# Kernel optimization log

Hardware: AMD Instinct MI355X
Metric: run time of the kernel (lower is better)

The kernel has to match this reference:

```python
import jax, jax.numpy as jnp
import numpy as np

B, S, H, HD = 2, 2048, 16, 128
HID = H * HD            # 2048
FF = 4 * HID            # 8192
ROT = int(HD * 0.25)    # 32 rotary dims (rotary_pct=0.25)
EPS = 1e-5
ROPE_BASE = 10000.0


def _layernorm(x, g, b):
    mu = jnp.mean(x, axis=-1, keepdims=True)
    var = jnp.mean(jnp.square(x - mu), axis=-1, keepdims=True)
    return (x - mu) * jax.lax.rsqrt(var + EPS) * g + b


def _rope_cos_sin(seq_len, dim, dtype):
    inv_freq = 1.0 / (ROPE_BASE ** (np.arange(0, dim, 2, dtype=np.float32) / dim))
    t = np.arange(seq_len, dtype=np.float32)
    freqs = np.outer(t, inv_freq)              # [S, dim/2]
    emb = np.concatenate([freqs, freqs], -1)   # [S, dim]
    return jnp.asarray(np.cos(emb), dtype), jnp.asarray(np.sin(emb), dtype)


def _apply_rope(x, cos, sin):
    # x: [B, H, S, ROT]; GPTNeoX rotate_half
    half = x.shape[-1] // 2
    x1, x2 = x[..., :half], x[..., half:]
    rot = jnp.concatenate([-x2, x1], axis=-1)
    return x * cos[None, None, :, :] + rot * sin[None, None, :, :]


def setup_inputs() -> dict:
    key = jax.random.key(0)
    ks = jax.random.split(key, 8)
    f = jnp.float32
    return {
        "hidden_states": jax.random.normal(ks[0], (B, S, HID), f),
        "ln1_g": jnp.ones((HID,), f), "ln1_b": jnp.zeros((HID,), f),
        "ln2_g": jnp.ones((HID,), f), "ln2_b": jnp.zeros((HID,), f),
        "W_qkv": jax.random.normal(ks[1], (HID, 3 * HID), f) * 0.02,
        "b_qkv": jnp.zeros((3 * HID,), f),
        "W_o": jax.random.normal(ks[2], (HID, HID), f) * 0.02,
        "b_o": jnp.zeros((HID,), f),
        "W_fc": jax.random.normal(ks[3], (HID, FF), f) * 0.02,
        "b_fc": jnp.zeros((FF,), f),
        "W_proj": jax.random.normal(ks[4], (FF, HID), f) * 0.02,
        "b_proj": jnp.zeros((HID,), f),
    }


def reference(hidden_states, ln1_g, ln1_b, ln2_g, ln2_b,
              W_qkv, b_qkv, W_o, b_o, W_fc, b_fc, W_proj, b_proj):
    dtype = hidden_states.dtype
    x = _layernorm(hidden_states, ln1_g, ln1_b)

    # fused QKV, GPTNeoX per-head interleaved layout [B,S,H,3*HD]
    qkv = (x @ W_qkv + b_qkv).reshape(B, S, H, 3 * HD)
    q = jnp.transpose(qkv[..., :HD], (0, 2, 1, 3))          # [B,H,S,HD]
    k = jnp.transpose(qkv[..., HD:2 * HD], (0, 2, 1, 3))
    v = jnp.transpose(qkv[..., 2 * HD:], (0, 2, 1, 3))

    cos, sin = _rope_cos_sin(S, ROT, dtype)
    q = jnp.concatenate([_apply_rope(q[..., :ROT], cos, sin), q[..., ROT:]], -1)
    k = jnp.concatenate([_apply_rope(k[..., :ROT], cos, sin), k[..., ROT:]], -1)

    # eager attention: scores / sqrt(hd), causal mask-fill, softmax, matmul
    scale = 1.0 / jnp.sqrt(jnp.asarray(HD, dtype))
    scores = jnp.einsum("bhqd,bhkd->bhqk", q, k) * scale
    causal = jnp.tril(jnp.ones((S, S), bool))
    scores = jnp.where(causal, scores, jnp.finfo(dtype).min)
    weights = jax.nn.softmax(scores, axis=-1)
    ctx = jnp.einsum("bhqk,bhkd->bhqd", weights, v)          # [B,H,S,HD]
    ctx = jnp.transpose(ctx, (0, 2, 1, 3)).reshape(B, S, HID)
    attn_out = ctx @ W_o + b_o

    # parallel residual: mlp(ln2(h)) + attn(ln1(h)) + h
    m = _layernorm(hidden_states, ln2_g, ln2_b)
    mlp_out = jax.nn.gelu(m @ W_fc + b_fc, approximate=False) @ W_proj + b_proj
    return mlp_out + attn_out + hidden_states
```

## Files before the change

### kernel.cpp

```cpp
#include <hip/hip_runtime.h>
#include <hip/hip_bf16.h>
#include <math.h>

#define BDIM 2
#define SDIM 2048
#define HDIM 16
#define HD 128
#define HID 2048
#define FFD 8192
#define NTOK (BDIM*SDIM)
#define QKVW (3*HID)

typedef __hip_bfloat16 bf16;
typedef __attribute__((ext_vector_type(8))) short short8;
typedef __attribute__((ext_vector_type(4))) short short4_;
typedef __attribute__((ext_vector_type(4))) float floatx4;

__device__ inline short bfbits(float f) {
  bf16 h = __float2bfloat16(f);
  short s;
  __builtin_memcpy(&s, &h, 2);
  return s;
}

__device__ inline float fast_erf(float x) {
  float ax = fabsf(x);
  float t = __builtin_amdgcn_rcpf(1.0f + 0.3275911f * ax);
  float p = t * (0.254829592f + t * (-0.284496736f + t * (1.421413741f
          + t * (-1.453152027f + t * 1.061405429f))));
  float e = __expf(-ax * ax);
  float r = 1.0f - p * e;
  return copysignf(r, x);
}

__global__ __launch_bounds__(256) void transpose_cvt(
    const float* __restrict__ W, bf16* __restrict__ Wt, int K, int N)
{
  __shared__ float tile[32][33];
  int n0 = blockIdx.x * 32, k0 = blockIdx.y * 32;
  int tx = threadIdx.x, ty = threadIdx.y;
  #pragma unroll
  for (int r = ty; r < 32; r += 8)
    tile[r][tx] = W[(size_t)(k0 + r) * N + n0 + tx];
  __syncthreads();
  #pragma unroll
  for (int r = ty; r < 32; r += 8)
    Wt[(size_t)(n0 + r) * K + k0 + tx] = __float2bfloat16(tile[tx][r]);
}

__global__ __launch_bounds__(256) void ln_both(
    const float* __restrict__ x,
    const float* __restrict__ g1, const float* __restrict__ b1,
    const float* __restrict__ g2, const float* __restrict__ b2,
    bf16* __restrict__ o1, bf16* __restrict__ o2)
{
  int row = blockIdx.x;
  int tid = threadIdx.x;
  const float4* xr = (const float4*)(x + (size_t)row * HID);
  float4 va = xr[tid], vb = xr[tid + 256];
  float s = va.x + va.y + va.z + va.w + vb.x + vb.y + vb.z + vb.w;
  float q = va.x*va.x + va.y*va.y + va.z*va.z + va.w*va.w
          + vb.x*vb.x + vb.y*vb.y + vb.z*vb.z + vb.w*vb.w;
  #pragma unroll
  for (int off = 1; off < 64; off <<= 1) {
    s += __shfl_xor(s, off);
    q += __shfl_xor(q, off);
  }
  __shared__ float red[8];
  int wave = tid >> 6;
  if ((tid & 63) == 0) { red[wave] = s; red[4 + wave] = q; }
  __syncthreads();
  s = red[0] + red[1] + red[2] + red[3];
  q = red[4] + red[5] + red[6] + red[7];
  float mu = s * (1.0f / HID);
  float var = q * (1.0f / HID) - mu * mu;
  float rs = rsqrtf(var + 1e-5f);

  const float4* g1v = (const float4*)g1; const float4* b1v = (const float4*)b1;
  const float4* g2v = (const float4*)g2; const float4* b2v = (const float4*)b2;
  short4_* o1v = (short4_*)(o1 + (size_t)row * HID);
  short4_* o2v = (short4_*)(o2 + (size_t)row * HID);
  #pragma unroll
  for (int p = 0; p < 2; ++p) {
    int e = tid + p * 256;
    float4 xv = (p == 0) ? va : vb;
    float4 gv = g1v[e], bv = b1v[e];
    short4_ pk;
    pk[0] = bfbits((xv.x - mu) * rs * gv.x + bv.x);
    pk[1] = bfbits((xv.y - mu) * rs * gv.y + bv.y);
    pk[2] = bfbits((xv.z - mu) * rs * gv.z + bv.z);
    pk[3] = bfbits((xv.w - mu) * rs * gv.w + bv.w);
    o1v[e] = pk;
    gv = g2v[e]; bv = b2v[e];
    pk[0] = bfbits((xv.x - mu) * rs * gv.x + bv.x);
    pk[1] = bfbits((xv.y - mu) * rs * gv.y + bv.y);
    pk[2] = bfbits((xv.z - mu) * rs * gv.z + bv.z);
    pk[3] = bfbits((xv.w - mu) * rs * gv.w + bv.w);
    o2v[e] = pk;
  }
}

template<int EPI, int BM>
__global__ __launch_bounds__(512, 2) void gemm2p(
    const bf16* __restrict__ A, const bf16* __restrict__ Bt,
    const float* __restrict__ bias,
    float* __restrict__ Cf, bf16* __restrict__ Cb,
    const bf16* __restrict__ r1b, const float* __restrict__ r2,
    int M, int N, int K)
{
  constexpr int NI = BM / 32;
  __shared__ bf16 SA[2][BM * 64];
  __shared__ bf16 SB[2][256 * 64];
  const int tid = threadIdx.x;
  const int wave = tid >> 6, lane = tid & 63;
  const int quad = lane >> 4, l16 = lane & 15;
  const int wr = wave >> 2, wc = wave & 3;
  const int n0 = blockIdx.x * 256, m0 = blockIdx.y * BM;

  const int stg_r = tid >> 3;
  const int stg_c = ((tid & 7) ^ ((tid >> 3) & 7)) << 3;
  const bf16* stgA = A + (size_t)(m0 + stg_r) * K + stg_c;
  const bf16* stgB = Bt + (size_t)(n0 + stg_r) * K + stg_c;

  floatx4 acc[NI][4];
  #pragma unroll
  for (int i = 0; i < NI; ++i)
    #pragma unroll
    for (int j = 0; j < 4; ++j) acc[i][j] = (floatx4)0.0f;

  const int KT = K >> 6;

#define STAGE_2P(KT1, BUF) {                                                   \
  const bf16* ga_ = stgA + (size_t)(KT1) * 64;                                 \
  const bf16* gb_ = stgB + (size_t)(KT1) * 64;                                 \
  _Pragma("unroll")                                                            \
  for (int s_ = 0; s_ < BM / 64; ++s_)                                         \
    __builtin_amdgcn_global_load_lds(                                          \
        (const __attribute__((address_space(1))) void*)(ga_ + (size_t)s_ * 64 * K), \
        (__attribute__((address_space(3))) void*)&SA[BUF][s_ * 4096 + wave * 512], 16, 0, 0); \
  _Pragma("unroll")                                                            \
  for (int s_ = 0; s_ < 4; ++s_)                                               \
    __builtin_amdgcn_global_load_lds(                                          \
        (const __attribute__((address_space(1))) void*)(gb_ + (size_t)s_ * 64 * K), \
        (__attribute__((address_space(3))) void*)&SB[BUF][s_ * 4096 + wave * 512], 16, 0, 0); }

  STAGE_2P(0, 0);
  __syncthreads();

  for (int kt = 0; kt < KT; ++kt) {
    const int cur = kt & 1;
    if (kt + 1 < KT) STAGE_2P(kt + 1, cur ^ 1);
    const bf16* as_ = &SA[cur][0];
    const bf16* bs_ = &SB[cur][0];
    #pragma unroll
    for (int kc = 0; kc < 2; ++kc) {
      const int csw = (((kc * 4 + quad) ^ (l16 & 7)) << 3);
      short8 av[NI], bv[4];
      #pragma unroll
      for (int i = 0; i < NI; ++i)
        av[i] = *(const short8*)&as_[(wr * (BM / 2) + i * 16 + l16) * 64 + csw];
      #pragma unroll
      for (int j = 0; j < 4; ++j)
        bv[j] = *(const short8*)&bs_[(wc * 64 + j * 16 + l16) * 64 + csw];
      #pragma unroll
      for (int i = 0; i < NI; ++i)
        #pragma unroll
        for (int j = 0; j < 4; ++j)
          acc[i][j] = __builtin_amdgcn_mfma_f32_16x16x32_bf16(av[i], bv[j], acc[i][j], 0, 0, 0);
    }
    __syncthreads();
  }
#undef STAGE_2P

  #pragma unroll
  for (int i = 0; i < NI; ++i) {
    #pragma unroll
    for (int j = 0; j < 4; ++j) {
      int col = n0 + wc * 64 + j * 16 + l16;
      float bsv = bias[col];
      #pragma unroll
      for (int r = 0; r < 4; ++r) {
        int row = m0 + wr * (BM / 2) + i * 16 + quad * 4 + r;
        size_t idx = (size_t)row * N + col;
        float v = acc[i][j][r] + bsv;
        if (EPI == 1) {
          v = 0.5f * v * (1.0f + fast_erf(v * 0.70710678118654752f));
          Cb[idx] = __float2bfloat16(v);
        } else if (EPI == 2) {
          Cf[idx] = v + __bfloat162float(r1b[idx]) + r2[idx];
        } else {
          Cb[idx] = __float2bfloat16(v);
        }
      }
    }
  }
}

__global__ __launch_bounds__(256) void rope_vt(
    bf16* __restrict__ qkv, bf16* __restrict__ vT)
{
  int bh = blockIdx.x, s0 = blockIdx.y * 32;
  int b = bh >> 4, h = bh & 15;
  int tid = threadIdx.x;
  __shared__ bf16 vs[32][136];
  const float qsc = 0.12751740f;

  for (int idx = tid; idx < 512; idx += 256) {
    int sl = idx >> 4, d = idx & 15;
    int s = s0 + sl;
    bf16* base = qkv + (size_t)(b * SDIM + s) * QKVW + h * 384;
    float fr = (float)s * expf(-(float)d * 0.5756462732485114f);
    float c = cosf(fr), sn = sinf(fr);
    float q1 = __bfloat162float(base[d]);
    float q2 = __bfloat162float(base[d + 16]);
    float k1 = __bfloat162float(base[128 + d]);
    float k2 = __bfloat162float(base[128 + d + 16]);
    base[d]        = __float2bfloat16(qsc * (q1 * c - q2 * sn));
    base[d + 16]   = __float2bfloat16(qsc * (q2 * c + q1 * sn));
    base[128 + d]      = __float2bfloat16(k1 * c - k2 * sn);
    base[128 + d + 16] = __float2bfloat16(k2 * c + k1 * sn);
  }
  for (int idx = tid; idx < 32 * 96; idx += 256) {
    int sl = idx / 96, d = 32 + idx % 96;
    bf16* base = qkv + (size_t)(b * SDIM + s0 + sl) * QKVW + h * 384;
    base[d] = __float2bfloat16(qsc * __bfloat162float(base[d]));
  }

  for (int idx = tid; idx < 32 * 128; idx += 256) {
    int sl = idx >> 7, d = idx & 127;
    vs[sl][d] = qkv[(size_t)(b * SDIM + s0 + sl) * QKVW + h * 384 + 256 + d];
  }
  __syncthreads();
  for (int idx = tid; idx < 32 * 128; idx += 256) {
    int d = idx >> 5, sl = idx & 31;
    vT[((size_t)bh * HD + d) * SDIM + s0 + sl] = vs[sl][d];
  }
}

#define LOAD_K(KB, K0) { \
  int krow_ = (K0); \
  _Pragma("unroll") for (int nh_ = 0; nh_ < 2; ++nh_) \
    _Pragma("unroll") for (int c_ = 0; c_ < 4; ++c_) \
      KB[nh_*4+c_] = *(const short8*)&Kb[(size_t)(krow_ + nh_*16 + l16) * QKVW + c_*32 + quad*8]; }

#define SOFTMAX(S0, S1, MR, LR, OO, ROWQ, DOMASK, K0, SLOT) { \
  if (DOMASK) { \
    _Pragma("unroll") for (int r_ = 0; r_ < 4; ++r_) { \
      int row_ = (ROWQ) + quad*4 + r_; \
      S0[r_] = ((K0) + l16 <= row_) ? S0[r_] : -1e30f; \
      S1[r_] = ((K0) + 16 + l16 <= row_) ? S1[r_] : -1e30f; } } \
  _Pragma("unroll") for (int r_ = 0; r_ < 4; ++r_) { \
    float mx_ = fmaxf(S0[r_], S1[r_]); \
    mx_ = fmaxf(mx_, __shfl_xor(mx_, 1)); \
    mx_ = fmaxf(mx_, __shfl_xor(mx_, 2)); \
    mx_ = fmaxf(mx_, __shfl_xor(mx_, 4)); \
    mx_ = fmaxf(mx_, __shfl_xor(mx_, 8)); \
    float mnew_ = fmaxf(MR[r_], mx_); \
    float alpha_ = __builtin_amdgcn_exp2f(MR[r_] - mnew_); \
    MR[r_] = mnew_; \
    S0[r_] = __builtin_amdgcn_exp2f(S0[r_] - mnew_); \
    S1[r_] = __builtin_amdgcn_exp2f(S1[r_] - mnew_); \
    float sm_ = S0[r_] + S1[r_]; \
    sm_ += __shfl_xor(sm_, 1); sm_ += __shfl_xor(sm_, 2); \
    sm_ += __shfl_xor(sm_, 4); sm_ += __shfl_xor(sm_, 8); \
    LR[r_] = LR[r_] * alpha_ + sm_; \
    _Pragma("unroll") for (int d_ = 0; d_ < 8; ++d_) OO[d_][r_] *= alpha_; \
    Ps[wave][SLOT][quad*4 + r_][l16]      = __float2bfloat16(S0[r_]); \
    Ps[wave][SLOT][quad*4 + r_][16 + l16] = __float2bfloat16(S1[r_]); } }

#define FLASH_ITER(IT, KC, KN) { \
  const int k0_ = (IT) * 32; \
  const int k0n_ = ((IT) + 1 < nk) ? k0_ + 32 : 0; \
  LOAD_K(KN, k0n_); \
  short8 vbuf_[8]; \
  _Pragma("unroll") for (int d_ = 0; d_ < 8; ++d_) \
    vbuf_[d_] = *(const short8*)&Vb[(size_t)(d_*16 + l16) * SDIM + k0_ + quad*8]; \
  floatx4 scB_[2]; scB_[0] = (floatx4)0.0f; scB_[1] = (floatx4)0.0f; \
  _Pragma("unroll") for (int c_ = 0; c_ < 4; ++c_) { \
    scB_[0] = __builtin_amdgcn_mfma_f32_16x16x32_bf16(aqB[c_], KC[c_],   scB_[0], 0,0,0); \
    scB_[1] = __builtin_amdgcn_mfma_f32_16x16x32_bf16(aqB[c_], KC[4+c_], scB_[1], 0,0,0); } \
  const bool actA_ = (k0_ <= qa + 15); \
  floatx4 scA_[2]; scA_[0] = (floatx4)0.0f; scA_[1] = (floatx4)0.0f; \
  if (actA_) { \
    _Pragma("unroll") for (int c_ = 0; c_ < 4; ++c_) { \
      scA_[0] = __builtin_amdgcn_mfma_f32_16x16x32_bf16(aqA[c_], KC[c_],   scA_[0], 0,0,0); \
      scA_[1] = __builtin_amdgcn_mfma_f32_16x16x32_bf16(aqA[c_], KC[4+c_], scA_[1], 0,0,0); } } \
  SOFTMAX(scB_[0], scB_[1], mB, lB, oB, qb, (k0_ + 32 >= kmax), k0_, 0); \
  if (actA_) { \
    SOFTMAX(scA_[0], scA_[1], mA, lA, oA, qa, (k0_ + 32 > qa + 15), k0_, 1); \
    short8 pfB_ = *(const short8*)&Ps[wave][0][l16][quad*8]; \
    short8 pfA_ = *(const short8*)&Ps[wave][1][l16][quad*8]; \
    _Pragma("unroll") for (int d_ = 0; d_ < 8; ++d_) { \
      oB[d_] = __builtin_amdgcn_mfma_f32_16x16x32_bf16(pfB_, vbuf_[d_], oB[d_], 0,0,0); \
      oA[d_] = __builtin_amdgcn_mfma_f32_16x16x32_bf16(pfA_, vbuf_[d_], oA[d_], 0,0,0); } \
  } else { \
    short8 pfB_ = *(const short8*)&Ps[wave][0][l16][quad*8]; \
    _Pragma("unroll") for (int d_ = 0; d_ < 8; ++d_) \
      oB[d_] = __builtin_amdgcn_mfma_f32_16x16x32_bf16(pfB_, vbuf_[d_], oB[d_], 0,0,0); } }

__global__ __launch_bounds__(256) void flash_attn(
    const bf16* __restrict__ qkv, const bf16* __restrict__ vT,
    bf16* __restrict__ ctx)
{
  int bh = blockIdx.x;
  int b = bh >> 4, h = bh & 15;
  int tid = threadIdx.x;
  int wave = tid >> 6, lane = tid & 63;
  int quad = lane >> 4, l16 = lane & 15;
  int p = blockIdx.y * 4 + wave;
  int qa = 16 * p;
  int qb = SDIM - 16 * (p + 1);
  int kmax = qb + 16;
  int nk = (kmax + 31) >> 5;
  const bf16* Qb = qkv + (size_t)b * SDIM * QKVW + h * 384;
  const bf16* Kb = Qb + 128;
  const bf16* Vb = vT + (size_t)bh * HD * SDIM;
  __shared__ bf16 Ps[4][2][16][32];

  short8 aqA[4], aqB[4];
  #pragma unroll
  for (int c = 0; c < 4; ++c) {
    aqA[c] = *(const short8*)&Qb[(size_t)(qa + l16) * QKVW + c * 32 + quad * 8];
    aqB[c] = *(const short8*)&Qb[(size_t)(qb + l16) * QKVW + c * 32 + quad * 8];
  }

  floatx4 oA[8], oB[8];
  #pragma unroll
  for (int d = 0; d < 8; ++d) { oA[d] = (floatx4)0.0f; oB[d] = (floatx4)0.0f; }
  float mA[4] = {-INFINITY, -INFINITY, -INFINITY, -INFINITY};
  float mB[4] = {-INFINITY, -INFINITY, -INFINITY, -INFINITY};
  float lA[4] = {0.0f, 0.0f, 0.0f, 0.0f};
  float lB[4] = {0.0f, 0.0f, 0.0f, 0.0f};

  short8 kb0[8], kb1[8];
  LOAD_K(kb0, 0);
  for (int it = 0; it < nk; it += 2) {
    FLASH_ITER(it, kb0, kb1);
    if (it + 1 < nk) { FLASH_ITER(it + 1, kb1, kb0); }
  }

  float rlA[4], rlB[4];
  #pragma unroll
  for (int r = 0; r < 4; ++r) { rlA[r] = 1.0f / lA[r]; rlB[r] = 1.0f / lB[r]; }
  #pragma unroll
  for (int d = 0; d < 8; ++d) {
    #pragma unroll
    for (int r = 0; r < 4; ++r) {
      int rowA = qa + quad * 4 + r;
      int rowB = qb + quad * 4 + r;
      ctx[((size_t)b * SDIM + rowA) * HID + h * HD + d * 16 + l16] =
          __float2bfloat16(oA[d][r] * rlA[r]);
      ctx[((size_t)b * SDIM + rowB) * HID + h * HD + d * 16 + l16] =
          __float2bfloat16(oB[d][r] * rlB[r]);
    }
  }
}

extern "C" void kernel_launch(void* const* d_in, const int* in_sizes, int n_in,
                              void* d_out, int out_size, void* d_ws, size_t ws_size,
                              hipStream_t stream) {
  const float* hidden = (const float*)d_in[0];
  const float* ln1g = (const float*)d_in[1];
  const float* ln1b = (const float*)d_in[2];
  const float* ln2g = (const float*)d_in[3];
  const float* ln2b = (const float*)d_in[4];
  const float* Wqkv = (const float*)d_in[5];
  const float* bqkv = (const float*)d_in[6];
  const float* Wo   = (const float*)d_in[7];
  const float* bo   = (const float*)d_in[8];
  const float* Wfc  = (const float*)d_in[9];
  const float* bfc  = (const float*)d_in[10];
  const float* Wproj= (const float*)d_in[11];
  const float* bproj= (const float*)d_in[12];

  char* ws = (char*)d_ws;
  const size_t SZ_WQKV = (size_t)QKVW * HID * 2;
  const size_t SZ_WO   = (size_t)HID * HID * 2;
  const size_t SZ_WFC  = (size_t)FFD * HID * 2;
  const size_t SZ_WPROJ= (size_t)HID * FFD * 2;
  const size_t SZ_ACT  = (size_t)NTOK * HID * 2;
  const size_t SZ_QKV  = (size_t)NTOK * QKVW * 2;

  bf16* wqkvT = (bf16*)(ws + 0);
  bf16* woT   = (bf16*)(ws + SZ_WQKV);
  bf16* wfcT  = (bf16*)(ws + SZ_WQKV + SZ_WO);
  bf16* wprojT= (bf16*)(ws + SZ_WQKV + SZ_WO + SZ_WFC);
  char* actbase = ws + SZ_WQKV + SZ_WO + SZ_WFC + SZ_WPROJ;
  bf16* xln   = (bf16*)(actbase);
  bf16* mln   = (bf16*)(actbase + SZ_ACT);
  bf16* qkvb  = (bf16*)(actbase + 2 * SZ_ACT);
  bf16* vT    = (bf16*)(actbase + 2 * SZ_ACT + SZ_QKV);
  bf16* ctx   = xln;
  bf16* attnb = wqkvT;
  bf16* hfc   = qkvb;

  dim3 tblk(32, 8);
  transpose_cvt<<<dim3(QKVW / 32, HID / 32), tblk, 0, stream>>>(Wqkv, wqkvT, HID, QKVW);
  transpose_cvt<<<dim3(HID / 32, HID / 32), tblk, 0, stream>>>(Wo, woT, HID, HID);
  transpose_cvt<<<dim3(FFD / 32, HID / 32), tblk, 0, stream>>>(Wfc, wfcT, HID, FFD);
  transpose_cvt<<<dim3(HID / 32, FFD / 32), tblk, 0, stream>>>(Wproj, wprojT, FFD, HID);

  ln_both<<<NTOK, 256, 0, stream>>>(hidden, ln1g, ln1b, ln2g, ln2b, xln, mln);

  gemm2p<3, 128><<<dim3(QKVW / 256, NTOK / 128), 512, 0, stream>>>(
      xln, wqkvT, bqkv, nullptr, qkvb, nullptr, nullptr, NTOK, QKVW, HID);

  rope_vt<<<dim3(32, SDIM / 32), 256, 0, stream>>>(qkvb, vT);

  flash_attn<<<dim3(32, SDIM / 128), 256, 0, stream>>>(qkvb, vT, ctx);

  gemm2p<3, 128><<<dim3(HID / 256, NTOK / 128), 512, 0, stream>>>(
      ctx, woT, bo, nullptr, attnb, nullptr, nullptr, NTOK, HID, HID);

  gemm2p<1, 256><<<dim3(FFD / 256, NTOK / 256), 512, 0, stream>>>(
      mln, wfcT, bfc, nullptr, hfc, nullptr, nullptr, NTOK, FFD, HID);

  gemm2p<2, 128><<<dim3(HID / 256, NTOK / 128), 512, 0, stream>>>(
      hfc, wprojT, bproj, (float*)d_out, nullptr, attnb, hidden, NTOK, HID, FFD);
}
```

Measured before the change: 1.036 ms.

## Give each flash-attention wave a single query tile instead of paired tiles

The attention kernel stops pairing a short and a long causal query tile per wave and now assigns one 16-row tile per wave, launching twice as many blocks in reverse order so the longest tiles start first. This halves per-wave register state (one set of accumulators and Q fragments), which allows a launch-bounds occupancy hint of 3 blocks per CU. In exchange, K/V loads are no longer shared between two query tiles, so global traffic per useful MFMA rises and load balance relies on the hardware scheduler rather than explicit pairing.

```diff
diff --git a/kernel.cpp b/kernel.cpp
--- a/kernel.cpp
+++ b/kernel.cpp
@@ -243,10 +243,10 @@
     _Pragma("unroll") for (int c_ = 0; c_ < 4; ++c_) \
       KB[nh_*4+c_] = *(const short8*)&Kb[(size_t)(krow_ + nh_*16 + l16) * QKVW + c_*32 + quad*8]; }
 
-#define SOFTMAX(S0, S1, MR, LR, OO, ROWQ, DOMASK, K0, SLOT) { \
+#define SOFTMAX1(S0, S1, K0, DOMASK) { \
   if (DOMASK) { \
     _Pragma("unroll") for (int r_ = 0; r_ < 4; ++r_) { \
-      int row_ = (ROWQ) + quad*4 + r_; \
+      int row_ = q0 + quad*4 + r_; \
       S0[r_] = ((K0) + l16 <= row_) ? S0[r_] : -1e30f; \
       S1[r_] = ((K0) + 16 + l16 <= row_) ? S1[r_] : -1e30f; } } \
   _Pragma("unroll") for (int r_ = 0; r_ < 4; ++r_) { \
@@ -255,50 +255,36 @@
     mx_ = fmaxf(mx_, __shfl_xor(mx_, 2)); \
     mx_ = fmaxf(mx_, __shfl_xor(mx_, 4)); \
     mx_ = fmaxf(mx_, __shfl_xor(mx_, 8)); \
-    float mnew_ = fmaxf(MR[r_], mx_); \
-    float alpha_ = __builtin_amdgcn_exp2f(MR[r_] - mnew_); \
-    MR[r_] = mnew_; \
+    float mnew_ = fmaxf(m[r_], mx_); \
+    float alpha_ = __builtin_amdgcn_exp2f(m[r_] - mnew_); \
+    m[r_] = mnew_; \
     S0[r_] = __builtin_amdgcn_exp2f(S0[r_] - mnew_); \
     S1[r_] = __builtin_amdgcn_exp2f(S1[r_] - mnew_); \
     float sm_ = S0[r_] + S1[r_]; \
     sm_ += __shfl_xor(sm_, 1); sm_ += __shfl_xor(sm_, 2); \
     sm_ += __shfl_xor(sm_, 4); sm_ += __shfl_xor(sm_, 8); \
-    LR[r_] = LR[r_] * alpha_ + sm_; \
-    _Pragma("unroll") for (int d_ = 0; d_ < 8; ++d_) OO[d_][r_] *= alpha_; \
-    Ps[wave][SLOT][quad*4 + r_][l16]      = __float2bfloat16(S0[r_]); \
-    Ps[wave][SLOT][quad*4 + r_][16 + l16] = __float2bfloat16(S1[r_]); } }
-
-#define FLASH_ITER(IT, KC, KN) { \
+    l[r_] = l[r_] * alpha_ + sm_; \
+    _Pragma("unroll") for (int d_ = 0; d_ < 8; ++d_) o[d_][r_] *= alpha_; \
+    Ps[wave][quad*4 + r_][l16]      = __float2bfloat16(S0[r_]); \
+    Ps[wave][quad*4 + r_][16 + l16] = __float2bfloat16(S1[r_]); } }
+
+#define FLASH_ITER1(IT, KC, KN) { \
   const int k0_ = (IT) * 32; \
   const int k0n_ = ((IT) + 1 < nk) ? k0_ + 32 : 0; \
   LOAD_K(KN, k0n_); \
   short8 vbuf_[8]; \
   _Pragma("unroll") for (int d_ = 0; d_ < 8; ++d_) \
     vbuf_[d_] = *(const short8*)&Vb[(size_t)(d_*16 + l16) * SDIM + k0_ + quad*8]; \
-  floatx4 scB_[2]; scB_[0] = (floatx4)0.0f; scB_[1] = (floatx4)0.0f; \
+  floatx4 sc_[2]; sc_[0] = (floatx4)0.0f; sc_[1] = (floatx4)0.0f; \
   _Pragma("unroll") for (int c_ = 0; c_ < 4; ++c_) { \
-    scB_[0] = __builtin_amdgcn_mfma_f32_16x16x32_bf16(aqB[c_], KC[c_],   scB_[0], 0,0,0); \
-    scB_[1] = __builtin_amdgcn_mfma_f32_16x16x32_bf16(aqB[c_], KC[4+c_], scB_[1], 0,0,0); } \
-  const bool actA_ = (k0_ <= qa + 15); \
-  floatx4 scA_[2]; scA_[0] = (floatx4)0.0f; scA_[1] = (floatx4)0.0f; \
-  if (actA_) { \
-    _Pragma("unroll") for (int c_ = 0; c_ < 4; ++c_) { \
-      scA_[0] = __builtin_amdgcn_mfma_f32_16x16x32_bf16(aqA[c_], KC[c_],   scA_[0], 0,0,0); \
-      scA_[1] = __builtin_amdgcn_mfma_f32_16x16x32_bf16(aqA[c_], KC[4+c_], scA_[1], 0,0,0); } } \
-  SOFTMAX(scB_[0], scB_[1], mB, lB, oB, qb, (k0_ + 32 >= kmax), k0_, 0); \
-  if (actA_) { \
-    SOFTMAX(scA_[0], scA_[1], mA, lA, oA, qa, (k0_ + 32 > qa + 15), k0_, 1); \
-    short8 pfB_ = *(const short8*)&Ps[wave][0][l16][quad*8]; \
-    short8 pfA_ = *(const short8*)&Ps[wave][1][l16][quad*8]; \
-    _Pragma("unroll") for (int d_ = 0; d_ < 8; ++d_) { \
-      oB[d_] = __builtin_amdgcn_mfma_f32_16x16x32_bf16(pfB_, vbuf_[d_], oB[d_], 0,0,0); \
-      oA[d_] = __builtin_amdgcn_mfma_f32_16x16x32_bf16(pfA_, vbuf_[d_], oA[d_], 0,0,0); } \
-  } else { \
-    short8 pfB_ = *(const short8*)&Ps[wave][0][l16][quad*8]; \
-    _Pragma("unroll") for (int d_ = 0; d_ < 8; ++d_) \
-      oB[d_] = __builtin_amdgcn_mfma_f32_16x16x32_bf16(pfB_, vbuf_[d_], oB[d_], 0,0,0); } }
-
-__global__ __launch_bounds__(256) void flash_attn(
+    sc_[0] = __builtin_amdgcn_mfma_f32_16x16x32_bf16(aq[c_], KC[c_],   sc_[0], 0,0,0); \
+    sc_[1] = __builtin_amdgcn_mfma_f32_16x16x32_bf16(aq[c_], KC[4+c_], sc_[1], 0,0,0); } \
+  SOFTMAX1(sc_[0], sc_[1], k0_, (k0_ + 32 >= kmax)); \
+  short8 pf_ = *(const short8*)&Ps[wave][l16][quad*8]; \
+  _Pragma("unroll") for (int d_ = 0; d_ < 8; ++d_) \
+    o[d_] = __builtin_amdgcn_mfma_f32_16x16x32_bf16(pf_, vbuf_[d_], o[d_], 0,0,0); }
+
+__global__ __launch_bounds__(256, 3) void flash_attn(
     const bf16* __restrict__ qkv, const bf16* __restrict__ vT,
     bf16* __restrict__ ctx)
 {
@@ -307,51 +293,43 @@
   int tid = threadIdx.x;
   int wave = tid >> 6, lane = tid & 63;
   int quad = lane >> 4, l16 = lane & 15;
-  int p = blockIdx.y * 4 + wave;
-  int qa = 16 * p;
-  int qb = SDIM - 16 * (p + 1);
-  int kmax = qb + 16;
+  int t = 127 - (blockIdx.y * 4 + wave);
+  int q0 = 16 * t;
+  int kmax = q0 + 16;
   int nk = (kmax + 31) >> 5;
   const bf16* Qb = qkv + (size_t)b * SDIM * QKVW + h * 384;
   const bf16* Kb = Qb + 128;
   const bf16* Vb = vT + (size_t)bh * HD * SDIM;
-  __shared__ bf16 Ps[4][2][16][32];
-
-  short8 aqA[4], aqB[4];
-  #pragma unroll
-  for (int c = 0; c < 4; ++c) {
-    aqA[c] = *(const short8*)&Qb[(size_t)(qa + l16) * QKVW + c * 32 + quad * 8];
-    aqB[c] = *(const short8*)&Qb[(size_t)(qb + l16) * QKVW + c * 32 + quad * 8];
-  }
-
-  floatx4 oA[8], oB[8];
-  #pragma unroll
-  for (int d = 0; d < 8; ++d) { oA[d] = (floatx4)0.0f; oB[d] = (floatx4)0.0f; }
-  float mA[4] = {-INFINITY, -INFINITY, -INFINITY, -INFINITY};
-  float mB[4] = {-INFINITY, -INFINITY, -INFINITY, -INFINITY};
-  float lA[4] = {0.0f, 0.0f, 0.0f, 0.0f};
-  float lB[4] = {0.0f, 0.0f, 0.0f, 0.0f};
+  __shared__ bf16 Ps[4][16][32];
+
+  short8 aq[4];
+  #pragma unroll
+  for (int c = 0; c < 4; ++c)
+    aq[c] = *(const short8*)&Qb[(size_t)(q0 + l16) * QKVW + c * 32 + quad * 8];
+
+  floatx4 o[8];
+  #pragma unroll
+  for (int d = 0; d < 8; ++d) o[d] = (floatx4)0.0f;
+  float m[4] = {-INFINITY, -INFINITY, -INFINITY, -INFINITY};
+  float l[4] = {0.0f, 0.0f, 0.0f, 0.0f};
 
   short8 kb0[8], kb1[8];
   LOAD_K(kb0, 0);
   for (int it = 0; it < nk; it += 2) {
-    FLASH_ITER(it, kb0, kb1);
-    if (it + 1 < nk) { FLASH_ITER(it + 1, kb1, kb0); }
-  }
-
-  float rlA[4], rlB[4];
-  #pragma unroll
-  for (int r = 0; r < 4; ++r) { rlA[r] = 1.0f / lA[r]; rlB[r] = 1.0f / lB[r]; }
+    FLASH_ITER1(it, kb0, kb1);
+    if (it + 1 < nk) { FLASH_ITER1(it + 1, kb1, kb0); }
+  }
+
+  float rl[4];
+  #pragma unroll
+  for (int r = 0; r < 4; ++r) rl[r] = 1.0f / l[r];
   #pragma unroll
   for (int d = 0; d < 8; ++d) {
     #pragma unroll
     for (int r = 0; r < 4; ++r) {
-      int rowA = qa + quad * 4 + r;
-      int rowB = qb + quad * 4 + r;
-      ctx[((size_t)b * SDIM + rowA) * HID + h * HD + d * 16 + l16] =
-          __float2bfloat16(oA[d][r] * rlA[r]);
-      ctx[((size_t)b * SDIM + rowB) * HID + h * HD + d * 16 + l16] =
-          __float2bfloat16(oB[d][r] * rlB[r]);
+      int row = q0 + quad * 4 + r;
+      ctx[((size_t)b * SDIM + row) * HID + h * HD + d * 16 + l16] =
+          __float2bfloat16(o[d][r] * rl[r]);
     }
   }
 }
@@ -407,7 +385,7 @@
 
   rope_vt<<<dim3(32, SDIM / 32), 256, 0, stream>>>(qkvb, vT);
 
-  flash_attn<<<dim3(32, SDIM / 128), 256, 0, stream>>>(qkvb, vT, ctx);
+  flash_attn<<<dim3(32, SDIM / 64), 256, 0, stream>>>(qkvb, vT, ctx);
 
   gemm2p<3, 128><<<dim3(HID / 256, NTOK / 128), 512, 0, stream>>>(
       ctx, woT, bo, nullptr, attnb, nullptr, nullptr, NTOK, HID, HID);
```

Result: slower. 1.267 ms (+22.3%).
